# Optimization experiments

Measured on AMD Instinct MI355X. Metric: run time of the kernel, lower is better.

## Reference

```python
import jax, jax.numpy as jnp
import numpy as np

S, B, H = 2048, 2, 2048
NH = 16
HD = H // NH  # 128
ROPE_BASE = 10000.0


def _rope_cos_sin(seq_len, dim, dtype):
    inv_freq = 1.0 / (ROPE_BASE ** (jnp.arange(0, dim, 2, dtype=jnp.float32) / dim))
    t = jnp.arange(seq_len, dtype=jnp.float32)
    freqs = jnp.outer(t, inv_freq)            # [S, dim/2]
    emb = jnp.concatenate([freqs, freqs], -1)  # [S, dim]
    return jnp.cos(emb).astype(dtype), jnp.sin(emb).astype(dtype)


def _rotate_half(x):
    x1, x2 = jnp.split(x, 2, axis=-1)
    return jnp.concatenate([-x2, x1], axis=-1)


def setup_inputs() -> dict:
    key = jax.random.key(0)
    k1, k2, k3 = jax.random.split(key, 3)
    hidden_states = jax.random.normal(k1, (S, B, H), dtype=jnp.float32)
    w_qkv = jax.random.normal(k2, (3 * H, H), dtype=jnp.float32) * (1.0 / np.sqrt(H))
    w_out = jax.random.normal(k3, (H, H), dtype=jnp.float32) * (1.0 / np.sqrt(H))
    return {"hidden_states": hidden_states, "w_qkv": w_qkv, "w_out": w_out}


def reference(hidden_states, w_qkv, w_out):
    seq_len, batch, _ = hidden_states.shape
    # QKV projection (nn.Linear: x @ W^T), bias=False
    qkv = jnp.einsum('sbh,oh->sbo', hidden_states, w_qkv)
    qkv = qkv.reshape(seq_len, batch, 3, NH, HD)
    q, k, v = qkv[:, :, 0], qkv[:, :, 1], qkv[:, :, 2]  # [S, B, NH, HD]

    cos, sin = _rope_cos_sin(seq_len, HD, hidden_states.dtype)
    cos = cos[:, None, None, :]
    sin = sin[:, None, None, :]
    q = q * cos + _rotate_half(q) * sin
    k = k * cos + _rotate_half(k) * sin

    # [S, B, NH, HD] -> [B, NH, S, HD]
    q = q.transpose(1, 2, 0, 3)
    k = k.transpose(1, 2, 0, 3)
    v = v.transpose(1, 2, 0, 3)

    scale = 1.0 / np.sqrt(HD)
    scores = jnp.einsum('bhqd,bhkd->bhqk', q, k) * scale
    causal = jnp.tril(jnp.ones((seq_len, seq_len), dtype=bool))
    scores = jnp.where(causal, scores, jnp.finfo(scores.dtype).min)
    probs = jax.nn.softmax(scores, axis=-1)
    attn = jnp.einsum('bhqk,bhkd->bhqd', probs, v)  # [B, NH, S, HD]

    # [B, NH, S, HD] -> [S, B, NH*HD]
    out = attn.transpose(2, 0, 1, 3).reshape(seq_len, batch, -1)
    out = jnp.einsum('sbh,oh->sbo', out, w_out)
    return out
```

## Files before the change

kernel.cpp:

```cpp
#include <hip/hip_runtime.h>
#include <hip/hip_bf16.h>

typedef __attribute__((ext_vector_type(8))) short bf16x8;
typedef __attribute__((ext_vector_type(8))) short s16x8;
typedef __attribute__((ext_vector_type(4))) float f32x4;
typedef __attribute__((ext_vector_type(4))) int i32x4;

#define SEQ 2048
#define BATCH 2
#define HID 2048
#define NH 16
#define HD 128
#define QKVN 6144

static __device__ __forceinline__ short f2bf(float f) {
    union { float f; unsigned u; } v; v.f = f;
    unsigned r = (v.u + 0x7FFFu + ((v.u >> 16) & 1u)) >> 16;
    return (short)r;
}

static __device__ __forceinline__ void gload_lds16(const short* g, short* l) {
    __builtin_amdgcn_global_load_lds((const __attribute__((address_space(1))) void*)g,
                                     (__attribute__((address_space(3))) void*)l, 16, 0, 0);
}

__global__ void cvt_kernel(const float* __restrict__ in, short* __restrict__ out, int n8) {
    const int i = blockIdx.x * 256 + threadIdx.x;
    if (i >= n8) return;
    f32x4 a = *(const f32x4*)(in + (size_t)i * 8);
    f32x4 b = *(const f32x4*)(in + (size_t)i * 8 + 4);
    s16x8 o = { f2bf(a.x), f2bf(a.y), f2bf(a.z), f2bf(a.w),
                f2bf(b.x), f2bf(b.y), f2bf(b.z), f2bf(b.w) };
    *(s16x8*)(out + (size_t)i * 8) = o;
}

#define STAGE_A(BUF, H, KK) do { \
    const short* _s = aSrc + (size_t)(H) * 64 * K + (KK) * 64; \
    short* _d = lds + (BUF) * 16384 + (H) * 8192 + w * 512; \
    gload_lds16(_s, _d); \
    gload_lds16(_s + (size_t)128 * K, _d + 4096); \
} while (0)

#define STAGE_B(BUF, H, KK) do { \
    const short* _s = bSrc + (size_t)(H) * 32 * K + (KK) * 64; \
    short* _d = lds + 32768 + (BUF) * 16384 + (H) * 8192 + w * 512; \
    gload_lds16(_s, _d); \
    gload_lds16(_s + (size_t)128 * K, _d + 4096); \
} while (0)

#define LOAD_A(MH) do { \
    const short* _p = lds + bufR * 16384 + (MH) * 8192 + aOff0; \
    const short* _q = lds + bufR * 16384 + (MH) * 8192 + aOff1; \
    _Pragma("unroll") \
    for (int mm = 0; mm < 4; ++mm) { \
        aR[mm][0] = *(const bf16x8*)(_p + mm * 1024); \
        aR[mm][1] = *(const bf16x8*)(_q + mm * 1024); \
    } \
} while (0)

#define LOAD_B(NHh) do { \
    const short* _p = lds + 32768 + bufR * 16384 + (NHh) * 8192 + bOff0; \
    const short* _q = lds + 32768 + bufR * 16384 + (NHh) * 8192 + bOff1; \
    _Pragma("unroll") \
    for (int nn = 0; nn < 2; ++nn) { \
        bR[(NHh) * 2 + nn][0] = *(const bf16x8*)(_p + nn * 1024); \
        bR[(NHh) * 2 + nn][1] = *(const bf16x8*)(_q + nn * 1024); \
    } \
} while (0)

#define MFMA_Q(MH, NHh) do { \
    _Pragma("unroll") \
    for (int mm = 0; mm < 4; ++mm) { \
        _Pragma("unroll") \
        for (int nn = 0; nn < 2; ++nn) { \
            f32x4 _c = acc[(MH) * 4 + mm][(NHh) * 2 + nn]; \
            _c = __builtin_amdgcn_mfma_f32_16x16x32_bf16(aR[mm][0], bR[(NHh) * 2 + nn][0], _c, 0, 0, 0); \
            _c = __builtin_amdgcn_mfma_f32_16x16x32_bf16(aR[mm][1], bR[(NHh) * 2 + nn][1], _c, 0, 0, 0); \
            acc[(MH) * 4 + mm][(NHh) * 2 + nn] = _c; \
        } \
    } \
} while (0)

__global__ __launch_bounds__(512, 2)
void gemm256(const short* __restrict__ A, const short* __restrict__ B,
             short* __restrict__ C, int N, int K) {
    __shared__ short lds[65536];

    const int tid = threadIdx.x;
    const int mBase = blockIdx.y * 256;
    const int nBase = blockIdx.x * 256;
    const int w = tid >> 6, lane = tid & 63, quad = lane >> 4, l15 = lane & 15;
    const int wm = w >> 2, wn = w & 3;

    const int kcol = 8 * ((tid & 7) ^ ((tid >> 3) & 7));
    const short* aSrc = A + (size_t)(mBase + (tid >> 3)) * K + kcol;
    const short* bSrc = B + (size_t)(nBase + ((tid >> 3) & 31) + ((tid >> 8) & 1) * 64) * K + kcol;

    const int cs0 = (quad * 8) ^ ((l15 & 7) << 3);
    const int aOff0 = (l15 + wm * 64) * 64 + cs0;
    const int aOff1 = aOff0 ^ 32;
    const int bOff0 = (l15 + wn * 32) * 64 + cs0;
    const int bOff1 = bOff0 ^ 32;

    const int NK = K >> 6;
    f32x4 acc[8][4] = {};
    bf16x8 aR[4][2], bR[4][2];

    STAGE_A(0, 0, 0); STAGE_B(0, 0, 0); STAGE_B(0, 1, 0); STAGE_A(0, 1, 0);
    STAGE_A(1, 0, 1); STAGE_B(1, 0, 1); STAGE_B(1, 1, 1);
    asm volatile("s_waitcnt vmcnt(6)" ::: "memory");
    __builtin_amdgcn_s_barrier();

    int bufR = 0;
    for (int k = 0; k < NK; ++k) {
        const int kk1 = (k + 1 < NK) ? k + 1 : NK - 1;
        const int kk2 = (k + 2 < NK) ? k + 2 : NK - 1;
        LOAD_A(0);
        LOAD_B(0);
        STAGE_A(bufR ^ 1, 1, kk1);
        asm volatile("s_waitcnt lgkmcnt(8)" ::: "memory");
        __builtin_amdgcn_s_barrier();
        asm volatile("s_waitcnt lgkmcnt(0)" ::: "memory");
        __builtin_amdgcn_s_setprio(1);
        MFMA_Q(0, 0);
        __builtin_amdgcn_s_setprio(0);
        __builtin_amdgcn_s_barrier();
        LOAD_B(1);
        STAGE_A(bufR, 0, kk2);
        __builtin_amdgcn_s_barrier();
        asm volatile("s_waitcnt lgkmcnt(0)" ::: "memory");
        __builtin_amdgcn_s_setprio(1);
        MFMA_Q(0, 1);
        __builtin_amdgcn_s_setprio(0);
        __builtin_amdgcn_s_barrier();
        LOAD_A(1);
        STAGE_B(bufR, 0, kk2);
        __builtin_amdgcn_s_barrier();
        asm volatile("s_waitcnt lgkmcnt(0)" ::: "memory");
        __builtin_amdgcn_s_setprio(1);
        MFMA_Q(1, 1);
        __builtin_amdgcn_s_setprio(0);
        __builtin_amdgcn_s_barrier();
        STAGE_B(bufR, 1, kk2);
        asm volatile("s_waitcnt vmcnt(6)" ::: "memory");
        __builtin_amdgcn_s_barrier();
        __builtin_amdgcn_s_setprio(1);
        MFMA_Q(1, 0);
        __builtin_amdgcn_s_setprio(0);
        __builtin_amdgcn_s_barrier();
        bufR ^= 1;
    }
    asm volatile("s_waitcnt vmcnt(0)" ::: "memory");

    #pragma unroll
    for (int f = 0; f < 8; ++f) {
        const int row0 = mBase + wm * 128 + f * 16 + quad * 4;
        #pragma unroll
        for (int g = 0; g < 4; ++g) {
            const int col = nBase + wn * 64 + g * 16 + l15;
            #pragma unroll
            for (int r = 0; r < 4; ++r)
                C[(size_t)(row0 + r) * N + col] = f2bf(acc[f][g][r]);
        }
    }
}

template<bool STORE_BF16>
__global__ __launch_bounds__(256, 2)
void gemm_bt(const short* __restrict__ A, const short* __restrict__ B,
             void* __restrict__ Cp, int N, int K) {
    __shared__ short As[128 * 32];
    __shared__ short Bs[128 * 32];

    const int tid = threadIdx.x;
    const int mBase = blockIdx.y * 128;
    const int nBase = blockIdx.x * 128;
    const int w = tid >> 6, lane = tid & 63, quad = lane >> 4, l15 = lane & 15;
    const int wr = (w >> 1) * 64, wc = (w & 1) * 64;

    const int r0 = tid >> 2;
    const int kc = (tid & 3) * 8;
    const short* aG = A + (size_t)(mBase + r0) * K + kc;
    const short* bG = B + (size_t)(nBase + r0) * K + kc;
    short* ldsA0 = As + w * 512;
    short* ldsA1 = As + 2048 + w * 512;
    short* ldsB0 = Bs + w * 512;
    short* ldsB1 = Bs + 2048 + w * 512;

    f32x4 acc[4][4] = {};

    for (int k0 = 0; k0 < K; k0 += 32) {
        __syncthreads();
        gload_lds16(aG + k0,                    ldsA0);
        gload_lds16(aG + (size_t)64 * K + k0,   ldsA1);
        gload_lds16(bG + k0,                    ldsB0);
        gload_lds16(bG + (size_t)64 * K + k0,   ldsB1);
        __syncthreads();

        bf16x8 af[4], bfb[4];
        #pragma unroll
        for (int i = 0; i < 4; ++i)
            af[i] = *(const bf16x8*)(As + (wr + i * 16 + l15) * 32 + quad * 8);
        #pragma unroll
        for (int j = 0; j < 4; ++j)
            bfb[j] = *(const bf16x8*)(Bs + (wc + j * 16 + l15) * 32 + quad * 8);
        #pragma unroll
        for (int i = 0; i < 4; ++i)
            #pragma unroll
            for (int j = 0; j < 4; ++j)
                acc[i][j] = __builtin_amdgcn_mfma_f32_16x16x32_bf16(af[i], bfb[j], acc[i][j], 0, 0, 0);
    }

    #pragma unroll
    for (int i = 0; i < 4; ++i) {
        const int row0 = mBase + wr + i * 16 + quad * 4;
        #pragma unroll
        for (int j = 0; j < 4; ++j) {
            const int col = nBase + wc + j * 16 + l15;
            #pragma unroll
            for (int r = 0; r < 4; ++r) {
                if (STORE_BF16)
                    ((short*)Cp)[(size_t)(row0 + r) * N + col] = f2bf(acc[i][j][r]);
                else
                    ((float*)Cp)[(size_t)(row0 + r) * N + col] = acc[i][j][r];
            }
        }
    }
}

__global__ void rope_kernel(short* __restrict__ qkv) {
    const int tid = blockIdx.x * 256 + threadIdx.x;
    const int d     = tid & 63;
    const int h     = (tid >> 6) & 15;
    const int which = (tid >> 10) & 1;
    const int b     = (tid >> 11) & 1;
    const int s     = tid >> 12;

    const size_t base = (size_t)(s * 2 + b) * QKVN + which * 2048 + h * 128;
    const float inv_freq = expf(-((float)(2 * d) * (1.0f / 128.0f)) * 9.210340371976184f);
    float sn, cs;
    sincosf((float)s * inv_freq, &sn, &cs);
    const float post = (which == 0) ? 0.08838834764831845f : 1.0f;

    union { unsigned u; float f; } x1, x2;
    x1.u = ((unsigned)(unsigned short)qkv[base + d]) << 16;
    x2.u = ((unsigned)(unsigned short)qkv[base + d + 64]) << 16;
    qkv[base + d]      = f2bf((x1.f * cs - x2.f * sn) * post);
    qkv[base + d + 64] = f2bf((x2.f * cs + x1.f * sn) * post);
}

__global__ void vtrans_kernel(const short* __restrict__ qkv, short* __restrict__ vT) {
    __shared__ short T[64][72];
    const int s0 = blockIdx.x * 64, d0 = blockIdx.y * 64;
    const int bh = blockIdx.z;
    const int b = bh >> 4, h = bh & 15;
    const int t = threadIdx.x;

    #pragma unroll
    for (int p = 0; p < 2; ++p) {
        const int sl = (t >> 3) + p * 32;
        const int dl = (t & 7) * 8;
        *(i32x4*)&T[sl][dl] =
            *(const i32x4*)(qkv + (size_t)((s0 + sl) * 2 + b) * QKVN + 4096 + h * 128 + d0 + dl);
    }
    __syncthreads();
    #pragma unroll
    for (int p = 0; p < 2; ++p) {
        const int dl = (t >> 3) + p * 32;
        const int sl = (t & 7) * 8;
        short tmp[8];
        #pragma unroll
        for (int j = 0; j < 8; ++j) tmp[j] = T[sl + j][dl];
        *(i32x4*)(vT + ((size_t)bh * 128 + d0 + dl) * 2048 + s0 + sl) = *(i32x4*)tmp;
    }
}

__global__ __launch_bounds__(256, 2)
void attn_kernel(const short* __restrict__ qkv, const short* __restrict__ vT,
                 short* __restrict__ out) {
    __shared__ short Kt[64][136];
    __shared__ short Vt[128][72];
    __shared__ short Ps[4][32][72];

    const int bx = blockIdx.x;
    const int h = blockIdx.y, b = blockIdx.z;
    const int Aq = (bx & 1) ? (bx >> 1) : (15 - (bx >> 1));
    const int qt = b ? (15 - Aq) : Aq;
    const int tid = threadIdx.x;
    const int w = tid >> 6, lane = tid & 63, quad = lane >> 4, l15 = lane & 15;

    bf16x8 aq[2][4];
    #pragma unroll
    for (int m = 0; m < 2; ++m) {
        const short* qbase =
            qkv + (size_t)((qt * 128 + w * 32 + m * 16 + l15) * 2 + b) * QKVN + h * 128;
        #pragma unroll
        for (int c = 0; c < 4; ++c)
            aq[m][c] = *(const bf16x8*)(qbase + c * 32 + quad * 8);
    }

    f32x4 oacc[2][8] = {};
    float lpart[2][4] = {};

    const int kRow = tid >> 2, kCol = (tid & 3) * 32;
    const int vRow = tid >> 1, vCol = (tid & 1) * 32;
    const short* kG = qkv + (size_t)b * QKVN + 2048 + h * 128 + kCol;
    const short* vG = vT + ((size_t)(b * 16 + h) * 128 + vRow) * 2048 + vCol;

    const int nChunks = 2 * qt + 2;

    for (int ck = 0; ck < nChunks; ++ck) {
        const int kk0 = ck * 64;
        __syncthreads();
        {
            const short* kp = kG + (size_t)(kk0 + kRow) * 2 * QKVN;
            const short* vp = vG + kk0;
            i32x4 kv[4], vv[4];
            #pragma unroll
            for (int i = 0; i < 4; ++i) kv[i] = *(const i32x4*)(kp + i * 8);
            #pragma unroll
            for (int i = 0; i < 4; ++i) vv[i] = *(const i32x4*)(vp + i * 8);
            #pragma unroll
            for (int i = 0; i < 4; ++i) *(i32x4*)&Kt[kRow][kCol + i * 8] = kv[i];
            #pragma unroll
            for (int i = 0; i < 4; ++i) *(i32x4*)&Vt[vRow][vCol + i * 8] = vv[i];
        }
        __syncthreads();

        f32x4 sc4[2][4] = {};
        #pragma unroll
        for (int c = 0; c < 4; ++c) {
            #pragma unroll
            for (int n = 0; n < 4; ++n) {
                bf16x8 bk = *(const bf16x8*)&Kt[n * 16 + l15][c * 32 + quad * 8];
                #pragma unroll
                for (int m = 0; m < 2; ++m)
                    sc4[m][n] = __builtin_amdgcn_mfma_f32_16x16x32_bf16(aq[m][c], bk, sc4[m][n], 0, 0, 0);
            }
        }

        const bool diag = (ck >= 2 * qt);
        #pragma unroll
        for (int m = 0; m < 2; ++m) {
            const int rowbase = qt * 128 + w * 32 + m * 16 + quad * 4;
            #pragma unroll
            for (int r = 0; r < 4; ++r) {
                #pragma unroll
                for (int n = 0; n < 4; ++n) {
                    float sv = sc4[m][n][r];
                    if (diag && (kk0 + n * 16 + l15 > rowbase + r)) sv = -1e30f;
                    const float p = __expf(sv);
                    lpart[m][r] += p;
                    Ps[w][m * 16 + quad * 4 + r][n * 16 + l15] = f2bf(p);
                }
            }
        }

        #pragma unroll
        for (int m = 0; m < 2; ++m) {
            #pragma unroll
            for (int kp2 = 0; kp2 < 2; ++kp2) {
                bf16x8 ap = *(const bf16x8*)&Ps[w][m * 16 + l15][kp2 * 32 + quad * 8];
                #pragma unroll
                for (int dt = 0; dt < 8; ++dt) {
                    bf16x8 bv = *(const bf16x8*)&Vt[dt * 16 + l15][kp2 * 32 + quad * 8];
                    oacc[m][dt] = __builtin_amdgcn_mfma_f32_16x16x32_bf16(ap, bv, oacc[m][dt], 0, 0, 0);
                }
            }
        }
    }

    #pragma unroll
    for (int m = 0; m < 2; ++m) {
        const int rowbase = qt * 128 + w * 32 + m * 16 + quad * 4;
        #pragma unroll
        for (int r = 0; r < 4; ++r) {
            float l = lpart[m][r];
            #pragma unroll
            for (int off = 1; off < 16; off <<= 1)
                l += __shfl_xor(l, off);
            const float inv_l = 1.0f / l;
            const size_t obase = (size_t)((rowbase + r) * 2 + b) * HID + h * 128;
            #pragma unroll
            for (int dt = 0; dt < 8; ++dt)
                out[obase + dt * 16 + l15] = f2bf(oacc[m][dt][r] * inv_l);
        }
    }
}

extern "C" void kernel_launch(void* const* d_in, const int* in_sizes, int n_in,
                              void* d_out, int out_size, void* d_ws, size_t ws_size,
                              hipStream_t stream) {
    const float* hidden = (const float*)d_in[0];
    const float* w_qkv  = (const float*)d_in[1];
    const float* w_out  = (const float*)d_in[2];
    float* out = (float*)d_out;

    short* qkv     = (short*)d_ws;
    short* attnb   = qkv + (size_t)4096 * QKVN;
    short* wqkv_bf = attnb + (size_t)4096 * HID;
    short* wout_bf = wqkv_bf;
    short* hbf     = wqkv_bf + (size_t)QKVN * HID;
    short* vT      = hbf;

    dim3 blk(256);
    cvt_kernel<<<dim3(4096), blk, 0, stream>>>(hidden, hbf, 4096 * 256);
    cvt_kernel<<<dim3(6144), blk, 0, stream>>>(w_qkv, wqkv_bf, 6144 * 256);
    gemm256<<<dim3(QKVN / 256, 4096 / 256), dim3(512), 0, stream>>>(
        hbf, wqkv_bf, qkv, QKVN, HID);
    cvt_kernel<<<dim3(2048), blk, 0, stream>>>(w_out, wout_bf, 2048 * 256);
    rope_kernel<<<dim3((SEQ * BATCH * 2 * NH * (HD / 2)) / 256), blk, 0, stream>>>(qkv);
    vtrans_kernel<<<dim3(SEQ / 64, HD / 64, BATCH * NH), blk, 0, stream>>>(qkv, vT);
    attn_kernel<<<dim3(SEQ / 128, NH, BATCH), blk, 0, stream>>>(qkv, vT, attnb);
    gemm_bt<false><<<dim3(HID / 128, 4096 / 128), blk, 0, stream>>>(
        attnb, wout_bf, out, HID, HID);
}
```

Measured before the change: 400.4 us.

## Double-buffer K/V tiles via direct global-to-LDS loads with XOR swizzle

```diff
diff --git a/kernel.cpp b/kernel.cpp
--- a/kernel.cpp
+++ b/kernel.cpp
@@ -278,9 +278,7 @@
 __global__ __launch_bounds__(256, 2)
 void attn_kernel(const short* __restrict__ qkv, const short* __restrict__ vT,
                  short* __restrict__ out) {
-    __shared__ short Kt[64][136];
-    __shared__ short Vt[128][72];
-    __shared__ short Ps[4][32][72];
+    __shared__ short lds[40960];
 
     const int bx = blockIdx.x;
     const int h = blockIdx.y, b = blockIdx.z;
@@ -288,6 +286,8 @@
     const int qt = b ? (15 - Aq) : Aq;
     const int tid = threadIdx.x;
     const int w = tid >> 6, lane = tid & 63, quad = lane >> 4, l15 = lane & 15;
+    const int bh = b * 16 + h;
+    const int cswz = (l15 & 7) << 3;
 
     bf16x8 aq[2][4];
     #pragma unroll
@@ -302,40 +302,53 @@
     f32x4 oacc[2][8] = {};
     float lpart[2][4] = {};
 
-    const int kRow = tid >> 2, kCol = (tid & 3) * 32;
-    const int vRow = tid >> 1, vCol = (tid & 1) * 32;
-    const short* kG = qkv + (size_t)b * QKVN + 2048 + h * 128 + kCol;
-    const short* vG = vT + ((size_t)(b * 16 + h) * 128 + vRow) * 2048 + vCol;
+    const short* kSrc0 = qkv + (size_t)((w * 16 + (lane >> 4)) * 2 + b) * QKVN
+                       + 2048 + h * 128 + ((lane & 15) ^ (lane >> 4)) * 8;
+    const short* kSrc1 = qkv + (size_t)((w * 16 + 4 + (lane >> 4)) * 2 + b) * QKVN
+                       + 2048 + h * 128 + ((lane & 15) ^ (4 | (lane >> 4))) * 8;
+    const short* vSrc = vT + ((size_t)bh * 128 + w * 32 + (lane >> 3)) * 2048
+                      + ((lane & 7) ^ ((lane >> 3) & 7)) * 8;
+    short* kDst = lds + w * 2048;
+    short* vDst = lds + 16384 + w * 2048;
+
+#define STAGE_KV(BUF, KK0) do { \
+    const size_t kAdv = (size_t)(KK0) * 2 * QKVN; \
+    short* _kd = kDst + (BUF) * 8192; \
+    short* _vd = vDst + (BUF) * 8192; \
+    gload_lds16(kSrc0 + kAdv,                  _kd); \
+    gload_lds16(kSrc1 + kAdv,                  _kd + 512); \
+    gload_lds16(kSrc0 + kAdv + 16 * QKVN,      _kd + 1024); \
+    gload_lds16(kSrc1 + kAdv + 16 * QKVN,      _kd + 1536); \
+    gload_lds16(vSrc + (KK0),                  _vd); \
+    gload_lds16(vSrc + (KK0) + 8 * 2048,       _vd + 512); \
+    gload_lds16(vSrc + (KK0) + 16 * 2048,      _vd + 1024); \
+    gload_lds16(vSrc + (KK0) + 24 * 2048,      _vd + 1536); \
+} while (0)
 
     const int nChunks = 2 * qt + 2;
 
+    STAGE_KV(0, 0);
+    asm volatile("s_waitcnt vmcnt(0)" ::: "memory");
+    __builtin_amdgcn_s_barrier();
+
     for (int ck = 0; ck < nChunks; ++ck) {
+        const int cur = ck & 1;
         const int kk0 = ck * 64;
-        __syncthreads();
-        {
-            const short* kp = kG + (size_t)(kk0 + kRow) * 2 * QKVN;
-            const short* vp = vG + kk0;
-            i32x4 kv[4], vv[4];
-            #pragma unroll
-            for (int i = 0; i < 4; ++i) kv[i] = *(const i32x4*)(kp + i * 8);
-            #pragma unroll
-            for (int i = 0; i < 4; ++i) vv[i] = *(const i32x4*)(vp + i * 8);
-            #pragma unroll
-            for (int i = 0; i < 4; ++i) *(i32x4*)&Kt[kRow][kCol + i * 8] = kv[i];
-            #pragma unroll
-            for (int i = 0; i < 4; ++i) *(i32x4*)&Vt[vRow][vCol + i * 8] = vv[i];
-        }
-        __syncthreads();
+        if (ck + 1 < nChunks) STAGE_KV(cur ^ 1, kk0 + 64);
+
+        const short* Kc = lds + cur * 8192;
+        const short* Vc = lds + 16384 + cur * 8192;
+        short* Pw = lds + 32768 + w * 2048;
 
         f32x4 sc4[2][4] = {};
         #pragma unroll
         for (int c = 0; c < 4; ++c) {
+            const int cb = (c * 32 + quad * 8) ^ cswz;
             #pragma unroll
             for (int n = 0; n < 4; ++n) {
-                bf16x8 bk = *(const bf16x8*)&Kt[n * 16 + l15][c * 32 + quad * 8];
-                #pragma unroll
-                for (int m = 0; m < 2; ++m)
-                    sc4[m][n] = __builtin_amdgcn_mfma_f32_16x16x32_bf16(aq[m][c], bk, sc4[m][n], 0, 0, 0);
+                bf16x8 bk = *(const bf16x8*)(Kc + (n * 16 + l15) * 128 + cb);
+                sc4[0][n] = __builtin_amdgcn_mfma_f32_16x16x32_bf16(aq[0][c], bk, sc4[0][n], 0, 0, 0);
+                sc4[1][n] = __builtin_amdgcn_mfma_f32_16x16x32_bf16(aq[1][c], bk, sc4[1][n], 0, 0, 0);
             }
         }
 
@@ -345,30 +358,36 @@
             const int rowbase = qt * 128 + w * 32 + m * 16 + quad * 4;
             #pragma unroll
             for (int r = 0; r < 4; ++r) {
+                const int prow = m * 16 + quad * 4 + r;
+                const int pswz = ((quad * 4 + r) & 7) << 3;
                 #pragma unroll
                 for (int n = 0; n < 4; ++n) {
                     float sv = sc4[m][n][r];
                     if (diag && (kk0 + n * 16 + l15 > rowbase + r)) sv = -1e30f;
                     const float p = __expf(sv);
                     lpart[m][r] += p;
-                    Ps[w][m * 16 + quad * 4 + r][n * 16 + l15] = f2bf(p);
+                    Pw[prow * 64 + ((n * 16 + l15) ^ pswz)] = f2bf(p);
                 }
             }
         }
 
         #pragma unroll
-        for (int m = 0; m < 2; ++m) {
-            #pragma unroll
-            for (int kp2 = 0; kp2 < 2; ++kp2) {
-                bf16x8 ap = *(const bf16x8*)&Ps[w][m * 16 + l15][kp2 * 32 + quad * 8];
-                #pragma unroll
-                for (int dt = 0; dt < 8; ++dt) {
-                    bf16x8 bv = *(const bf16x8*)&Vt[dt * 16 + l15][kp2 * 32 + quad * 8];
-                    oacc[m][dt] = __builtin_amdgcn_mfma_f32_16x16x32_bf16(ap, bv, oacc[m][dt], 0, 0, 0);
-                }
+        for (int kp2 = 0; kp2 < 2; ++kp2) {
+            const int cb = (kp2 * 32 + quad * 8) ^ cswz;
+            bf16x8 ap0 = *(const bf16x8*)(Pw + l15 * 64 + cb);
+            bf16x8 ap1 = *(const bf16x8*)(Pw + (16 + l15) * 64 + cb);
+            #pragma unroll
+            for (int dt = 0; dt < 8; ++dt) {
+                bf16x8 bv = *(const bf16x8*)(Vc + (dt * 16 + l15) * 64 + cb);
+                oacc[0][dt] = __builtin_amdgcn_mfma_f32_16x16x32_bf16(ap0, bv, oacc[0][dt], 0, 0, 0);
+                oacc[1][dt] = __builtin_amdgcn_mfma_f32_16x16x32_bf16(ap1, bv, oacc[1][dt], 0, 0, 0);
             }
         }
-    }
+
+        asm volatile("s_waitcnt vmcnt(0)" ::: "memory");
+        __builtin_amdgcn_s_barrier();
+    }
+#undef STAGE_KV
 
     #pragma unroll
     for (int m = 0; m < 2; ++m) {
```

Measured after the change: 387.4 us. 3.2% less time.
